# Performance work log

Measured on AMD Instinct MI355X. Metric: run time of the kernel, lower is better.

Reference implementation:

```python
import jax, jax.numpy as jnp
import numpy as np

NH = 8  # num_heads


def _conv1x1(w, b, x):
    # 1x1 conv == channel matmul: w [O,C], x [B,C,H,W]
    return jnp.einsum('oc,bchw->bohw', w, x) + b[None, :, None, None]


def _fwd(low_freq_feat, high_freq_feat, ext_context, road_feat,
         ext_proj_w, ext_proj_b, road_proj_w, road_proj_b,
         ext_qkv_w, ext_qkv_b, road_qkv_w, road_qkv_b,
         ext_out_w, ext_out_b, road_out_w, road_out_b,
         gate_ext_w, gate_ext_b, gate_road_w, gate_road_b):
    B, C, H, W = low_freq_feat.shape
    nh = NH
    hd = C // nh
    HW = H * W
    scale = hd ** -0.5

    ext_p = ext_context @ ext_proj_w.T + ext_proj_b          # [B,C]
    road_p = _conv1x1(road_proj_w, road_proj_b, road_feat)   # [B,C,H,W]

    eqkv = (ext_p @ ext_qkv_w.T + ext_qkv_b).reshape(B, 3, nh, hd)
    ext_q, ext_v = eqkv[:, 0], eqkv[:, 2]                    # [B,nh,hd]

    # torch: conv out [B,3C,H,W] viewed as (B,C,3,H,W) -> q/k/v interleaved over channels
    rqkv = _conv1x1(road_qkv_w, road_qkv_b, road_p).reshape(B, C, 3, H, W)
    road_k = rqkv[:, :, 1].reshape(B, nh, hd, HW).transpose(0, 1, 3, 2)  # [B,nh,HW,hd]
    road_v = rqkv[:, :, 2].reshape(B, nh, hd, HW).transpose(0, 1, 3, 2)

    # ext->road attention. The torch code expands ext_q to HW identical rows; one row
    # per (batch, head) gives a bit-identical result without the [B,nh,HW,HW] blowup.
    scores = jnp.einsum('bnd,bnpd->bnp', ext_q, road_k) * scale
    attn = jax.nn.softmax(scores, axis=-1)                   # [B,nh,HW]
    ext_head = jnp.einsum('bnp,bnpd->bnd', attn, road_v).reshape(B, C)
    ext_vec = ext_head @ ext_out_w.T + ext_out_b             # [B,C]
    ext_feat_spatial = jnp.broadcast_to(ext_vec[:, :, None, None], (B, C, H, W))

    # road->ext attention: all HW keys/values are copies of the single ext token, so
    # softmax is exactly uniform and the output per position is exactly ext_v. The
    # road_out 1x1 conv on a spatially-constant map is a single matvec per batch.
    road_vec = ext_v.reshape(B, C) @ road_out_w.T + road_out_b
    road_enhanced = jnp.broadcast_to(road_vec[:, :, None, None], (B, C, H, W))

    # gated fusion (ext stream): spatial mean of constant map == ext_vec
    gate_in = jnp.concatenate([low_freq_feat.mean(axis=(2, 3)), ext_vec], axis=-1)
    ext_gate = jax.nn.sigmoid(gate_in @ gate_ext_w.T + gate_ext_b)[:, :, None, None]
    ext_final = low_freq_feat * (1.0 - ext_gate) + ext_feat_spatial * ext_gate

    # gated fusion (road stream)
    rg_in = jnp.concatenate([high_freq_feat, road_enhanced], axis=1)  # [B,2C,H,W]
    road_gate = jax.nn.sigmoid(_conv1x1(gate_road_w, gate_road_b, rg_in))
    road_final = high_freq_feat * (1.0 - road_gate) + road_enhanced * road_gate
    return ext_final, road_final


def setup_inputs() -> dict:
    key = jax.random.key(0)
    ks = jax.random.split(key, 20)
    B, C, H, W, E = 8, 256, 64, 64, 64
    f = lambda k, shape, s=1.0: jax.random.normal(k, shape, dtype=jnp.float32) * s
    return {
        'low_freq_feat': f(ks[0], (B, C, H, W)),
        'high_freq_feat': f(ks[1], (B, C, H, W)),
        'ext_context': f(ks[2], (B, E)),
        'road_feat': f(ks[3], (B, C, H, W)),
        'ext_proj_w': f(ks[4], (C, E), 0.05), 'ext_proj_b': f(ks[5], (C,), 0.02),
        'road_proj_w': f(ks[6], (C, C), 0.05), 'road_proj_b': f(ks[7], (C,), 0.02),
        'ext_qkv_w': f(ks[8], (3 * C, C), 0.05), 'ext_qkv_b': f(ks[9], (3 * C,), 0.02),
        'road_qkv_w': f(ks[10], (3 * C, C), 0.05), 'road_qkv_b': f(ks[11], (3 * C,), 0.02),
        'ext_out_w': f(ks[12], (C, C), 0.05), 'ext_out_b': f(ks[13], (C,), 0.02),
        'road_out_w': f(ks[14], (C, C), 0.05), 'road_out_b': f(ks[15], (C,), 0.02),
        'gate_ext_w': f(ks[16], (C, 2 * C), 0.05), 'gate_ext_b': f(ks[17], (C,), 0.02),
        'gate_road_w': f(ks[18], (C, 2 * C), 0.05), 'gate_road_b': f(ks[19], (C,), 0.02),
    }


def reference(low_freq_feat, high_freq_feat, ext_context, road_feat,
              ext_proj_w, ext_proj_b, road_proj_w, road_proj_b,
              ext_qkv_w, ext_qkv_b, road_qkv_w, road_qkv_b,
              ext_out_w, ext_out_b, road_out_w, road_out_b,
              gate_ext_w, gate_ext_b, gate_road_w, gate_road_b):
    return _fwd(low_freq_feat, high_freq_feat, ext_context, road_feat,
                ext_proj_w, ext_proj_b, road_proj_w, road_proj_b,
                ext_qkv_w, ext_qkv_b, road_qkv_w, road_qkv_b,
                ext_out_w, ext_out_b, road_out_w, road_out_b,
                gate_ext_w, gate_ext_b, gate_road_w, gate_road_b)
```

## Files before the change

kernel.cpp:

```cpp
#include <hip/hip_runtime.h>

typedef short bf16x8 __attribute__((ext_vector_type(8)));
typedef float f32x4 __attribute__((ext_vector_type(4)));

#define ATT_SCALE 0.17677669529663687f

__device__ __forceinline__ unsigned short f2b(float f) {
    unsigned int u = __builtin_bit_cast(unsigned int, f);
    unsigned int r = u + 0x7FFFu + ((u >> 16) & 1u);
    return (unsigned short)(r >> 16);
}
__device__ __forceinline__ float b2f(unsigned short v) {
    return __builtin_bit_cast(float, (unsigned int)v << 16);
}
__device__ __forceinline__ float wsum64(float v) {
    #pragma unroll
    for (int m = 32; m; m >>= 1) v += __shfl_xor(v, m, 64);
    return v;
}


__global__ __launch_bounds__(256) void k_setup(const float* __restrict__ w1,
                                               const float* __restrict__ wqkv,
                                               const float* __restrict__ b1,
                                               const float* __restrict__ bqkv,
                                               const float* __restrict__ gate_road_w,
                                               const float* __restrict__ ext_proj_w,
                                               const float* __restrict__ ext_qkv_w,
                                               const float* __restrict__ road_out_w,
                                               const float* __restrict__ ext_out_w,
                                               const float* __restrict__ gate_ext_w,
                                               const float* __restrict__ low,
                                               unsigned short* __restrict__ W3b,
                                               unsigned short* __restrict__ Wcb,
                                               unsigned short* __restrict__ WF,
                                               float* __restrict__ bcv,
                                               float* __restrict__ mean_low) {
    int bid = blockIdx.x, t = threadIdx.x;
    __shared__ float sel[8][256];
    __shared__ float red[8][4];
    if (bid >= 448) {
        int bc = bid - 448;
        const f32x4* p4 = (const f32x4*)(low + (size_t)bc * 4096);
        float s = 0.f;
        for (int i = t; i < 1024; i += 256) {
            f32x4 v = p4[i];
            s += v[0] + v[1] + v[2] + v[3];
        }
        s = wsum64(s);
        if ((t & 63) == 0) red[0][t >> 6] = s;
        __syncthreads();
        if (t == 0) mean_low[bc] = (red[0][0] + red[0][1] + red[0][2] + red[0][3]) * (1.0f / 4096.0f);
    } else if (bid < 256) {
        int i = bid * 256 + t;
        int o = i >> 8, k = i & 255;
        W3b[i] = f2b(gate_road_w[o * 512 + k]);
    } else if (bid < 320) {
        int o0 = (bid - 256) * 8;
        #pragma unroll
        for (int r = 0; r < 8; r++) {
            int o = o0 + r;
            int c = (o < 256) ? o : o - 256;
            int g = (o < 256) ? 1 : 2;
            sel[r][t] = wqkv[(size_t)(3 * c + g) * 256 + t];
        }
        __syncthreads();
        float b1v = b1[t];
        #pragma unroll
        for (int r = 0; r < 8; r++) {
            float v = wsum64(sel[r][t] * b1v);
            if ((t & 63) == 0) red[r][t >> 6] = v;
        }
        __syncthreads();
        if (t < 8) {
            int o = o0 + t;
            int c = (o < 256) ? o : o - 256;
            int g = (o < 256) ? 1 : 2;
            bcv[o] = red[t][0] + red[t][1] + red[t][2] + red[t][3] + bqkv[3 * c + g];
        }
        float acc[8] = {};
        #pragma unroll 16
        for (int m = 0; m < 256; m++) {
            float w1v = w1[(size_t)m * 256 + t];
            #pragma unroll
            for (int r = 0; r < 8; r++) acc[r] += sel[r][m] * w1v;
        }
        #pragma unroll
        for (int r = 0; r < 8; r++) Wcb[(size_t)(o0 + r) * 256 + t] = f2b(acc[r]);
    } else {
        int mb = bid - 320;
        int m = mb >> 4, ctile = mb & 15;
        const float* src;
        int stride, K, coff;
        unsigned short* dst;
        switch (m) {
        case 0: src = ext_qkv_w;                     stride = 256; K = 256; coff = 0;   dst = WF;          break;
        case 1: src = ext_qkv_w + (size_t)512 * 256; stride = 256; K = 256; coff = 0;   dst = WF + 65536;  break;
        case 2: src = road_out_w;                    stride = 256; K = 256; coff = 0;   dst = WF + 131072; break;
        case 3: src = gate_road_w;                   stride = 512; K = 256; coff = 256; dst = WF + 196608; break;
        case 4: src = ext_proj_w;                    stride = 64;  K = 64;  coff = 0;   dst = WF + 262144; break;
        case 5: src = ext_out_w;                     stride = 256; K = 256; coff = 0;   dst = WF + 278528; break;
        case 6: src = gate_ext_w;                    stride = 512; K = 256; coff = 0;   dst = WF + 344064; break;
        default: src = gate_ext_w;                   stride = 512; K = 256; coff = 256; dst = WF + 409600; break;
        }
        int lc = t >> 4, kseg = t & 15;
        int k0 = kseg * 16;
        if (k0 < K) {
            int c = ctile * 16 + lc;
            const float* sp = src + (size_t)c * stride + coff + k0;
            f32x4 v0 = *(const f32x4*)sp;
            f32x4 v1 = *(const f32x4*)(sp + 4);
            f32x4 v2 = *(const f32x4*)(sp + 8);
            f32x4 v3 = *(const f32x4*)(sp + 12);
            int kk = kseg >> 1;
            int Kt = K >> 5;
            #pragma unroll
            for (int h = 0; h < 2; h++) {
                int lhi = (kseg & 1) * 2 + h;
                int lane = lhi * 16 + lc;
                bf16x8 o;
                f32x4 a = h ? v2 : v0, b = h ? v3 : v1;
                #pragma unroll
                for (int i = 0; i < 4; i++) { o[i] = (short)f2b(a[i]); o[4 + i] = (short)f2b(b[i]); }
                *(bf16x8*)(dst + ((size_t)(ctile * Kt + kk) << 9) + lane * 8) = o;
            }
        }
    }
}

__global__ __launch_bounds__(256) void k_tiny(const unsigned short* __restrict__ WF,
                                              const float* __restrict__ ext_context,
                                              const float* __restrict__ ext_proj_b,
                                              const float* __restrict__ ext_qkv_b,
                                              const float* __restrict__ road_out_b,
                                              const float* __restrict__ gate_road_b,
                                              float* __restrict__ ext_q,
                                              float* __restrict__ road_vec,
                                              float* __restrict__ rg_const) {
    __shared__ unsigned short xA[16][264];
    __shared__ unsigned short xB[16][264];
    int t = threadIdx.x;
    int w = t >> 6, lane = t & 63, l15 = lane & 15, lhi = lane >> 4;
    const unsigned short* WqF  = WF;
    const unsigned short* WvF  = WF + 65536;
    const unsigned short* WroF = WF + 131072;
    const unsigned short* WgF  = WF + 196608;
    const unsigned short* WpF  = WF + 262144;
    {
        int b = t >> 5, k0 = (t & 31) * 2;
        float c0v = ext_context[b * 64 + k0];
        float c1v = ext_context[b * 64 + k0 + 1];
        *(unsigned int*)&xA[b][k0] = (unsigned int)f2b(c0v) | ((unsigned int)f2b(c1v) << 16);
    }
    __syncthreads();
    {
        f32x4 acc[4] = {};
        #pragma unroll
        for (int kk = 0; kk < 2; kk++) {
            bf16x8 a = *(const bf16x8*)&xA[l15][kk * 32 + 8 * lhi];
            #pragma unroll
            for (int ni = 0; ni < 4; ni++) {
                int ct = w * 4 + ni;
                bf16x8 bfr = *(const bf16x8*)(WpF + ((size_t)(ct * 2 + kk) << 9) + lane * 8);
                acc[ni] = __builtin_amdgcn_mfma_f32_16x16x32_bf16(a, bfr, acc[ni], 0, 0, 0);
            }
        }
        if (lhi < 2) {
            #pragma unroll
            for (int ni = 0; ni < 4; ni++) {
                int c = w * 64 + ni * 16 + l15;
                float bp = ext_proj_b[c];
                #pragma unroll
                for (int r = 0; r < 4; r++)
                    xB[4 * lhi + r][c] = f2b(acc[ni][r] + bp);
            }
        }
    }
    __syncthreads();
    {
        f32x4 acc[8] = {};
        bool isq = (w < 2);
        int cbase = (w & 1) * 128;
        const unsigned short* Wb = isq ? WqF : WvF;
        for (int kk = 0; kk < 8; kk++) {
            bf16x8 a = *(const bf16x8*)&xB[l15][kk * 32 + 8 * lhi];
            #pragma unroll
            for (int ni = 0; ni < 8; ni++) {
                int ct = (cbase >> 4) + ni;
                bf16x8 bfr = *(const bf16x8*)(Wb + ((size_t)(ct * 8 + kk) << 9) + lane * 8);
                acc[ni] = __builtin_amdgcn_mfma_f32_16x16x32_bf16(a, bfr, acc[ni], 0, 0, 0);
            }
        }
        if (lhi < 2) {
            #pragma unroll
            for (int ni = 0; ni < 8; ni++) {
                int c = cbase + ni * 16 + l15;
                float bb = ext_qkv_b[(isq ? 0 : 512) + c];
                #pragma unroll
                for (int r = 0; r < 4; r++) {
                    int b = 4 * lhi + r;
                    float val = acc[ni][r] + bb;
                    if (isq) ext_q[b * 256 + c] = val;
                    else     xA[b][c] = f2b(val);
                }
            }
        }
    }
    __syncthreads();
    {
        f32x4 acc[4] = {};
        for (int kk = 0; kk < 8; kk++) {
            bf16x8 a = *(const bf16x8*)&xA[l15][kk * 32 + 8 * lhi];
            #pragma unroll
            for (int ni = 0; ni < 4; ni++) {
                int ct = w * 4 + ni;
                bf16x8 bfr = *(const bf16x8*)(WroF + ((size_t)(ct * 8 + kk) << 9) + lane * 8);
                acc[ni] = __builtin_amdgcn_mfma_f32_16x16x32_bf16(a, bfr, acc[ni], 0, 0, 0);
            }
        }
        if (lhi < 2) {
            #pragma unroll
            for (int ni = 0; ni < 4; ni++) {
                int c = w * 64 + ni * 16 + l15;
                float bb = road_out_b[c];
                #pragma unroll
                for (int r = 0; r < 4; r++) {
                    int b = 4 * lhi + r;
                    float val = acc[ni][r] + bb;
                    road_vec[b * 256 + c] = val;
                    xB[b][c] = f2b(val);
                }
            }
        }
    }
    __syncthreads();
    {
        f32x4 acc[4] = {};
        for (int kk = 0; kk < 8; kk++) {
            bf16x8 a = *(const bf16x8*)&xB[l15][kk * 32 + 8 * lhi];
            #pragma unroll
            for (int ni = 0; ni < 4; ni++) {
                int ct = w * 4 + ni;
                bf16x8 bfr = *(const bf16x8*)(WgF + ((size_t)(ct * 8 + kk) << 9) + lane * 8);
                acc[ni] = __builtin_amdgcn_mfma_f32_16x16x32_bf16(a, bfr, acc[ni], 0, 0, 0);
            }
        }
        if (lhi < 2) {
            #pragma unroll
            for (int ni = 0; ni < 4; ni++) {
                int c = w * 64 + ni * 16 + l15;
                float bb = gate_road_b[c];
                #pragma unroll
                for (int r = 0; r < 4; r++)
                    rg_const[(4 * lhi + r) * 256 + c] = acc[ni][r] + bb;
            }
        }
    }
}

__global__ __launch_bounds__(256) void k_qfold(const unsigned short* __restrict__ Wcb,
                                               const float* __restrict__ bcv,
                                               const float* __restrict__ ext_q,
                                               unsigned short* __restrict__ wqf,
                                               float* __restrict__ cqs) {
    int b = blockIdx.x, t = threadIdx.x;
    __shared__ float qs[256];
    __shared__ float wq[8][256];
    qs[t] = ext_q[b * 256 + t];
    __syncthreads();
    float acc[8] = {};
    #pragma unroll
    for (int h = 0; h < 8; h++)
        #pragma unroll 8
        for (int d = 0; d < 32; d++)
            acc[h] += qs[h * 32 + d] * b2f(Wcb[(size_t)(h * 32 + d) * 256 + t]);
    #pragma unroll
    for (int h = 0; h < 8; h++) wq[h][t] = acc[h];
    if (t < 8) {
        float s = 0.f;
        #pragma unroll 8
        for (int d = 0; d < 32; d++) s += qs[t * 32 + d] * bcv[t * 32 + d];
        cqs[b * 8 + t] = s * ATT_SCALE;
    }
    __syncthreads();
    #pragma unroll
    for (int q2 = 0; q2 < 2; q2++) {
        int idx = t + 256 * q2;
        int kk = idx >> 6, l = idx & 63;
        int row = l & 15;
        int kb = kk * 32 + (l >> 4) * 8;
        bf16x8 o;
        #pragma unroll
        for (int e = 0; e < 8; e++)
            o[e] = (row < 8) ? (short)f2b(wq[row][kb + e]) : (short)0;
        *(bf16x8*)(wqf + ((size_t)(b * 8 + kk) * 64 + l) * 8) = o;
    }
}

__global__ __launch_bounds__(256) void k_att(const float* __restrict__ road_feat,
                                             const unsigned short* __restrict__ wqf,
                                             const float* __restrict__ cqs,
                                             float* __restrict__ part) {
    __shared__ unsigned short Xs[32 * 256];
    __shared__ unsigned short Xt[256][40];
    __shared__ float es_[8][36];
    __shared__ float Yl[256 * 12];
    char* Xc = (char*)Xs;
    int bid = blockIdx.x;
    int b  = bid >> 7;
    int p0 = (bid & 127) << 5;
    int t  = threadIdx.x;
    const float* rfb = road_feat + (size_t)b * 1048576;

    int c0 = 2 * (t >> 3);
    int j4 = (t & 7) * 4;
    #pragma unroll
    for (int it = 0; it < 4; ++it) {
        int c = c0 + 64 * it;
        f32x4 g0 = *(const f32x4*)(rfb + (size_t)c * 4096 + p0 + j4);
        f32x4 g1 = *(const f32x4*)(rfb + (size_t)(c + 1) * 4096 + p0 + j4);
        unsigned short h0[4], h1[4];
        #pragma unroll
        for (int i = 0; i < 4; i++) { h0[i] = f2b(g0[i]); h1[i] = f2b(g1[i]); }
        #pragma unroll
        for (int i = 0; i < 4; i++) {
            int j = j4 + i;
            unsigned int pk = (unsigned int)h0[i] | ((unsigned int)h1[i] << 16);
            *(unsigned int*)(Xc + ((j * 512 + 2 * c) ^ ((j & 15) << 4))) = pk;
        }
        *(unsigned int*)&Xt[c][j4]         = (unsigned int)h0[0] | ((unsigned int)h0[1] << 16);
        *(unsigned int*)&Xt[c][j4 + 2]     = (unsigned int)h0[2] | ((unsigned int)h0[3] << 16);
        *(unsigned int*)&Xt[c + 1][j4]     = (unsigned int)h1[0] | ((unsigned int)h1[1] << 16);
        *(unsigned int*)&Xt[c + 1][j4 + 2] = (unsigned int)h1[2] | ((unsigned int)h1[3] << 16);
    }
    __syncthreads();

    int w = t >> 6, lane = t & 63, l15 = lane & 15, lhi = lane >> 4;

    if (w < 2) {
        f32x4 acc = {};
        int px = w * 16 + l15;
        for (int kk = 0; kk < 8; kk++) {
            bf16x8 aq = *(const bf16x8*)(wqf + ((size_t)(b * 8 + kk) * 64 + lane) * 8);
            bf16x8 bx = *(const bf16x8*)(Xc + ((px * 512 + (kk * 32 + 8 * lhi) * 2) ^ ((px & 15) << 4)));
            acc = __builtin_amdgcn_mfma_f32_16x16x32_bf16(aq, bx, acc, 0, 0, 0);
        }
        #pragma unroll
        for (int r = 0; r < 4; r++) {
            int row = 4 * lhi + r;
            if (row < 8)
                es_[row][w * 16 + l15] = expf(acc[r] * ATT_SCALE + cqs[b * 8 + row]);
        }
    }
    __syncthreads();

    float* pb = part + (size_t)bid * 2056;
    {
        float v = es_[t >> 5][t & 31];
        v += __shfl_xor(v, 1, 64);
        v += __shfl_xor(v, 2, 64);
        v += __shfl_xor(v, 4, 64);
        v += __shfl_xor(v, 8, 64);
        v += __shfl_xor(v, 16, 64);
        if ((lane & 31) == 0) pb[t >> 5] = v;
    }
    bf16x8 besv;
    {
        f32x4 e0 = *(const f32x4*)&es_[l15 & 7][8 * lhi];
        f32x4 e1 = *(const f32x4*)&es_[l15 & 7][8 * lhi + 4];
        #pragma unroll
        for (int i = 0; i < 4; i++) { besv[i] = (short)f2b(e0[i]); besv[4 + i] = (short)f2b(e1[i]); }
    }
    #pragma unroll
    for (int mf = 0; mf < 4; mf++) {
        int f = w * 4 + mf;
        int c = f * 16 + l15;
        bf16x8 ax = *(const bf16x8*)&Xt[c][8 * lhi];
        f32x4 acc = {};
        acc = __builtin_amdgcn_mfma_f32_16x16x32_bf16(ax, besv, acc, 0, 0, 0);
        if (l15 < 8) {
            #pragma unroll
            for (int r = 0; r < 4; r++)
                Yl[(f * 16 + 4 * lhi + r) * 12 + l15] = acc[r];
        }
    }
    __syncthreads();
    {
        f32x4 y0, y1;
        #pragma unroll
        for (int i = 0; i < 4; i++) { y0[i] = Yl[t * 12 + i]; y1[i] = Yl[t * 12 + 4 + i]; }
        *(f32x4*)(pb + 8 + t * 8)     = y0;
        *(f32x4*)(pb + 8 + t * 8 + 4) = y1;
    }
}

__global__ __launch_bounds__(256) void k_red(const float* __restrict__ part,
                                             float* __restrict__ part2) {
    int blk = blockIdx.x, t = threadIdx.x;
    int base = blk * 8;
    float acc[8] = {};
    float accS = 0.f;
    #pragma unroll
    for (int g = 0; g < 8; g++) {
        const float* pb = part + (size_t)(base + g) * 2056;
        #pragma unroll
        for (int i = 0; i < 8; i++) acc[i] += pb[8 + 256 * i + t];
        if (t < 8) accS += pb[t];
    }
    float* ob = part2 + (size_t)blk * 2056;
    if (t < 8) ob[t] = accS;
    #pragma unroll
    for (int i = 0; i < 8; i++) ob[8 + 256 * i + t] = acc[i];
}

__global__ __launch_bounds__(256) void k_comb(const float* __restrict__ part2,
                                              const unsigned short* __restrict__ Wcb,
                                              const float* __restrict__ bcv,
                                              float* __restrict__ hdg) {
    int b = blockIdx.x, t = threadIdx.x;
    __shared__ float Yt[8][260];
    __shared__ float S[8];
    const float* pbase = part2 + (size_t)b * 16 * 2056;
    float acc[8] = {};
    float accS = 0.f;
    #pragma unroll 4
    for (int g = 0; g < 16; g++) {
        const float* pb = pbase + (size_t)g * 2056;
        #pragma unroll
        for (int i = 0; i < 8; i++) acc[i] += pb[8 + 256 * i + t];
        if (t < 8) accS += pb[t];
    }
    #pragma unroll
    for (int i = 0; i < 8; i++) {
        int e = 256 * i + t;
        Yt[e & 7][e >> 3] = acc[i];
    }
    if (t < 8) S[t] = accS;
    __syncthreads();

    int w = t >> 6, lane = t & 63, l15 = lane & 15, lhi = lane >> 4;
    float invS = 1.0f / S[l15 & 7];
    #pragma unroll
    for (int mf = 0; mf < 4; mf++) {
        int f = w * 4 + mf;
        f32x4 acc4 = {};
        for (int kk = 0; kk < 8; kk++) {
            bf16x8 aw = *(const bf16x8*)(Wcb + (size_t)(256 + f * 16 + l15) * 256 + kk * 32 + 8 * lhi);
            f32x4 y0 = *(const f32x4*)&Yt[l15 & 7][kk * 32 + 8 * lhi];
            f32x4 y1 = *(const f32x4*)&Yt[l15 & 7][kk * 32 + 8 * lhi + 4];
            bf16x8 by;
            #pragma unroll
            for (int i = 0; i < 4; i++) { by[i] = (short)f2b(y0[i]); by[4 + i] = (short)f2b(y1[i]); }
            acc4 = __builtin_amdgcn_mfma_f32_16x16x32_bf16(aw, by, acc4, 0, 0, 0);
        }
        if (l15 == (f >> 1)) {
            #pragma unroll
            for (int r = 0; r < 4; r++) {
                int row = f * 16 + 4 * lhi + r;
                hdg[b * 256 + row] = acc4[r] * invS + bcv[256 + row];
            }
        }
    }
}

__global__ __launch_bounds__(256) void k_vec2(const unsigned short* __restrict__ WF,
                                              const float* __restrict__ hdg,
                                              const float* __restrict__ mean_low,
                                              const float* __restrict__ ext_out_b,
                                              const float* __restrict__ gate_ext_b,
                                              float* __restrict__ ext_vec,
                                              float* __restrict__ ext_gate) {
    __shared__ unsigned short xA[16][264];
    __shared__ unsigned short xB[16][264];
    __shared__ unsigned short xC[16][264];
    int t = threadIdx.x;
    int w = t >> 6, lane = t & 63, l15 = lane & 15, lhi = lane >> 4;
    const unsigned short* WoF    = WF + 278528;
    const unsigned short* WgeLoF = WF + 344064;
    const unsigned short* WgeHiF = WF + 409600;
    {
        int bb = t >> 5, kb = t & 31;
        #pragma unroll
        for (int q = 0; q < 4; q++) {
            int k0 = (kb + 32 * q) * 2;
            *(unsigned int*)&xA[bb][k0] =
                (unsigned int)f2b(hdg[bb * 256 + k0]) | ((unsigned int)f2b(hdg[bb * 256 + k0 + 1]) << 16);
            *(unsigned int*)&xB[bb][k0] =
                (unsigned int)f2b(mean_low[bb * 256 + k0]) | ((unsigned int)f2b(mean_low[bb * 256 + k0 + 1]) << 16);
        }
    }
    __syncthreads();
    {
        f32x4 acc[4] = {};
        for (int kk = 0; kk < 8; kk++) {
            bf16x8 a = *(const bf16x8*)&xA[l15][kk * 32 + 8 * lhi];
            #pragma unroll
            for (int ni = 0; ni < 4; ni++) {
                int ct = w * 4 + ni;
                bf16x8 bfr = *(const bf16x8*)(WoF + ((size_t)(ct * 8 + kk) << 9) + lane * 8);
                acc[ni] = __builtin_amdgcn_mfma_f32_16x16x32_bf16(a, bfr, acc[ni], 0, 0, 0);
            }
        }
        if (lhi < 2) {
            #pragma unroll
            for (int ni = 0; ni < 4; ni++) {
                int c = w * 64 + ni * 16 + l15;
                float bb = ext_out_b[c];
                #pragma unroll
                for (int r = 0; r < 4; r++) {
                    int b = 4 * lhi + r;
                    float val = acc[ni][r] + bb;
                    ext_vec[b * 256 + c] = val;
                    xC[b][c] = f2b(val);
                }
            }
        }
    }
    __syncthreads();
    {
        f32x4 acc[4] = {};
        for (int kk = 0; kk < 8; kk++) {
            bf16x8 a = *(const bf16x8*)&xB[l15][kk * 32 + 8 * lhi];
            #pragma unroll
            for (int ni = 0; ni < 4; ni++) {
                int ct = w * 4 + ni;
                bf16x8 bfr = *(const bf16x8*)(WgeLoF + ((size_t)(ct * 8 + kk) << 9) + lane * 8);
                acc[ni] = __builtin_amdgcn_mfma_f32_16x16x32_bf16(a, bfr, acc[ni], 0, 0, 0);
            }
        }
        for (int kk = 0; kk < 8; kk++) {
            bf16x8 a = *(const bf16x8*)&xC[l15][kk * 32 + 8 * lhi];
            #pragma unroll
            for (int ni = 0; ni < 4; ni++) {
                int ct = w * 4 + ni;
                bf16x8 bfr = *(const bf16x8*)(WgeHiF + ((size_t)(ct * 8 + kk) << 9) + lane * 8);
                acc[ni] = __builtin_amdgcn_mfma_f32_16x16x32_bf16(a, bfr, acc[ni], 0, 0, 0);
            }
        }
        if (lhi < 2) {
            #pragma unroll
            for (int ni = 0; ni < 4; ni++) {
                int c = w * 64 + ni * 16 + l15;
                float bb = gate_ext_b[c];
                #pragma unroll
                for (int r = 0; r < 4; r++) {
                    int b = 4 * lhi + r;
                    ext_gate[b * 256 + c] = 1.0f / (1.0f + expf(-(acc[ni][r] + bb)));
                }
            }
        }
    }
}

__global__ __launch_bounds__(256) void k_ext_final(const float* __restrict__ low,
                                                   const float* __restrict__ ext_vec,
                                                   const float* __restrict__ ext_gate,
                                                   float* __restrict__ out) {
    int idx = blockIdx.x * 256 + threadIdx.x;
    #pragma unroll
    for (int rep = 0; rep < 4; ++rep) {
        int i = idx + rep * 524288;
        int bc = i >> 10;
        float g = ext_gate[bc];
        float vv = ext_vec[bc];
        f32x4 L = *(const f32x4*)(low + (size_t)i * 4);
        f32x4 o;
        #pragma unroll
        for (int c = 0; c < 4; c++) o[c] = L[c] + g * (vv - L[c]);
        *(f32x4*)(out + (size_t)i * 4) = o;
    }
}

__global__ __launch_bounds__(512) void k_road(const float* __restrict__ high,
                                              const unsigned short* __restrict__ W3b,
                                              const float* __restrict__ rg_const,
                                              const float* __restrict__ road_vec,
                                              float* __restrict__ outbuf) {
    __shared__ float Xs[32 * 256];
    char* Xc = (char*)Xs;
    int bid = blockIdx.x;
    int b  = bid >> 7;
    int p0 = (bid & 127) << 5;
    int t  = threadIdx.x;
    const float* hb = high + (size_t)b * 1048576;

    int c0 = t >> 3;
    int j4 = (t & 7) * 4;
    #pragma unroll
    for (int it = 0; it < 4; ++it) {
        int c = c0 + 64 * it;
        f32x4 g = *(const f32x4*)(hb + (size_t)c * 4096 + p0 + j4);
        #pragma unroll
        for (int i = 0; i < 4; i++) {
            int j = j4 + i;
            *(float*)(Xc + ((j * 1024 + 4 * c) ^ ((j & 15) << 4))) = g[i];
        }
    }
    __syncthreads();

    int w = t >> 6, lane = t & 63, l15 = lane & 15, lhi = lane >> 4;
    f32x4 acc[2][2] = {};
    for (int kk = 0; kk < 8; kk++) {
        bf16x8 a[2];
        #pragma unroll
        for (int mi = 0; mi < 2; mi++) {
            int j = mi * 16 + l15;
            int base = j * 1024 + (kk * 32 + 8 * lhi) * 4;
            int sw = (j & 15) << 4;
            f32x4 x0 = *(const f32x4*)(Xc + (base ^ sw));
            f32x4 x1 = *(const f32x4*)(Xc + ((base + 16) ^ sw));
            bf16x8 av;
            #pragma unroll
            for (int i = 0; i < 4; i++) {
                av[i]     = (short)f2b(x0[i]);
                av[4 + i] = (short)f2b(x1[i]);
            }
            a[mi] = av;
        }
        #pragma unroll
        for (int ni = 0; ni < 2; ni++) {
            int o = w * 32 + ni * 16 + l15;
            bf16x8 bf = *(const bf16x8*)(W3b + (size_t)o * 256 + kk * 32 + 8 * lhi);
            acc[0][ni] = __builtin_amdgcn_mfma_f32_16x16x32_bf16(a[0], bf, acc[0][ni], 0, 0, 0);
            acc[1][ni] = __builtin_amdgcn_mfma_f32_16x16x32_bf16(a[1], bf, acc[1][ni], 0, 0, 0);
        }
    }
    __syncthreads();

    #pragma unroll
    for (int ni = 0; ni < 2; ni++) {
        int o = w * 32 + ni * 16 + l15;
        float rc = rg_const[b * 256 + o];
        float rv = road_vec[b * 256 + o];
        #pragma unroll
        for (int mi = 0; mi < 2; mi++)
            #pragma unroll
            for (int r = 0; r < 4; r++) {
                int j = mi * 16 + 4 * lhi + r;
                float* slot = (float*)(Xc + ((j * 1024 + 4 * o) ^ ((j & 15) << 4)));
                float z = acc[mi][ni][r] + rc;
                float gte = 1.0f / (1.0f + expf(-z));
                float hv = *slot;
                *slot = hv + gte * (rv - hv);
            }
    }
    __syncthreads();

    float* ob = outbuf + 8388608 + (size_t)b * 1048576;
    #pragma unroll
    for (int it = 0; it < 4; ++it) {
        int c = c0 + 64 * it;
        f32x4 o4;
        #pragma unroll
        for (int i = 0; i < 4; i++) {
            int j = j4 + i;
            o4[i] = *(const float*)(Xc + ((j * 1024 + 4 * c) ^ ((j & 15) << 4)));
        }
        *(f32x4*)(ob + (size_t)c * 4096 + p0 + j4) = o4;
    }
}

extern "C" void kernel_launch(void* const* d_in, const int* in_sizes, int n_in,
                              void* d_out, int out_size, void* d_ws, size_t ws_size,
                              hipStream_t stream) {
    const float* low         = (const float*)d_in[0];
    const float* high        = (const float*)d_in[1];
    const float* ext_context = (const float*)d_in[2];
    const float* road_feat   = (const float*)d_in[3];
    const float* ext_proj_w  = (const float*)d_in[4];
    const float* ext_proj_b  = (const float*)d_in[5];
    const float* road_proj_w = (const float*)d_in[6];
    const float* road_proj_b = (const float*)d_in[7];
    const float* ext_qkv_w   = (const float*)d_in[8];
    const float* ext_qkv_b   = (const float*)d_in[9];
    const float* road_qkv_w  = (const float*)d_in[10];
    const float* road_qkv_b  = (const float*)d_in[11];
    const float* ext_out_w   = (const float*)d_in[12];
    const float* ext_out_b   = (const float*)d_in[13];
    const float* road_out_w  = (const float*)d_in[14];
    const float* road_out_b  = (const float*)d_in[15];
    const float* gate_ext_w  = (const float*)d_in[16];
    const float* gate_ext_b  = (const float*)d_in[17];
    const float* gate_road_w = (const float*)d_in[18];
    const float* gate_road_b = (const float*)d_in[19];

    float* out = (float*)d_out;
    unsigned short* wsb = (unsigned short*)d_ws;
    unsigned short* Wcb = wsb;
    unsigned short* W3b = wsb + 131072;
    float* fw = (float*)((char*)d_ws + 983040);
    float* ext_q    = fw;
    float* road_vec = fw + 2048;
    float* rg_const = fw + 4096;
    float* ext_vec  = fw + 8192;
    float* ext_gate = fw + 10240;
    float* mean_low = fw + 12288;
    float* bcv      = fw + 14336;
    float* hdg      = fw + 16384;
    float* cqs      = fw + 18432;
    unsigned short* wqf = (unsigned short*)(fw + 18496);
    float* part  = out + 2097152;
    float* part2 = out + 4718592;
    unsigned short* WF = (unsigned short*)(out + 5242880);

    k_setup<<<2496, 256, 0, stream>>>(road_proj_w, road_qkv_w, road_proj_b, road_qkv_b,
                                      gate_road_w, ext_proj_w, ext_qkv_w, road_out_w,
                                      ext_out_w, gate_ext_w, low,
                                      W3b, Wcb, WF, bcv, mean_low);
    k_tiny<<<1, 256, 0, stream>>>(WF, ext_context, ext_proj_b, ext_qkv_b,
                                  road_out_b, gate_road_b, ext_q, road_vec, rg_const);
    k_qfold<<<8, 256, 0, stream>>>(Wcb, bcv, ext_q, wqf, cqs);
    k_att<<<1024, 256, 0, stream>>>(road_feat, wqf, cqs, part);
    k_red<<<128, 256, 0, stream>>>(part, part2);
    k_comb<<<8, 256, 0, stream>>>(part2, Wcb, bcv, hdg);
    k_vec2<<<1, 256, 0, stream>>>(WF, hdg, mean_low, ext_out_b, gate_ext_b,
                                  ext_vec, ext_gate);
    k_ext_final<<<2048, 256, 0, stream>>>(low, ext_vec, ext_gate, out);
    k_road<<<1024, 512, 0, stream>>>(high, W3b, rg_const, road_vec, out);
}
```

Baseline: 149.0 us.

## Shrink k_road tiles to 16 positions and alias k_att shared buffers

k_road now runs 2048 blocks of 256 threads, each handling 16 spatial positions instead of 32, with each wave covering 64 output channels over a single M tile. This halves the LDS footprint per block so more blocks can be resident per CU. k_att aliases its Yl scratch onto the Xs staging buffer to cut LDS use and raise occupancy. The trade-off is that each W3b fragment loaded from global memory is reused across fewer positions, so weight traffic per output goes up.

```diff
diff --git a/kernel.cpp b/kernel.cpp
--- a/kernel.cpp
+++ b/kernel.cpp
@@ -301,11 +301,11 @@
                                              const unsigned short* __restrict__ wqf,
                                              const float* __restrict__ cqs,
                                              float* __restrict__ part) {
-    __shared__ unsigned short Xs[32 * 256];
+    __shared__ __align__(16) char u_smem[32 * 256 * 2];
     __shared__ unsigned short Xt[256][40];
     __shared__ float es_[8][36];
-    __shared__ float Yl[256 * 12];
-    char* Xc = (char*)Xs;
+    char* Xc = u_smem;
+    float* Yl = (float*)u_smem;
     int bid = blockIdx.x;
     int b  = bid >> 7;
     int p0 = (bid & 127) << 5;
@@ -571,21 +571,21 @@
     }
 }
 
-__global__ __launch_bounds__(512) void k_road(const float* __restrict__ high,
+__global__ __launch_bounds__(256) void k_road(const float* __restrict__ high,
                                               const unsigned short* __restrict__ W3b,
                                               const float* __restrict__ rg_const,
                                               const float* __restrict__ road_vec,
                                               float* __restrict__ outbuf) {
-    __shared__ float Xs[32 * 256];
+    __shared__ float Xs[16 * 256];
     char* Xc = (char*)Xs;
     int bid = blockIdx.x;
-    int b  = bid >> 7;
-    int p0 = (bid & 127) << 5;
+    int b  = bid >> 8;
+    int p0 = (bid & 255) << 4;
     int t  = threadIdx.x;
     const float* hb = high + (size_t)b * 1048576;
 
-    int c0 = t >> 3;
-    int j4 = (t & 7) * 4;
+    int c0 = t >> 2;
+    int j4 = (t & 3) * 4;
     #pragma unroll
     for (int it = 0; it < 4; ++it) {
         int c = c0 + 64 * it;
@@ -599,50 +599,41 @@
     __syncthreads();
 
     int w = t >> 6, lane = t & 63, l15 = lane & 15, lhi = lane >> 4;
-    f32x4 acc[2][2] = {};
+    f32x4 acc[4] = {};
     for (int kk = 0; kk < 8; kk++) {
-        bf16x8 a[2];
-        #pragma unroll
-        for (int mi = 0; mi < 2; mi++) {
-            int j = mi * 16 + l15;
-            int base = j * 1024 + (kk * 32 + 8 * lhi) * 4;
-            int sw = (j & 15) << 4;
-            f32x4 x0 = *(const f32x4*)(Xc + (base ^ sw));
-            f32x4 x1 = *(const f32x4*)(Xc + ((base + 16) ^ sw));
-            bf16x8 av;
-            #pragma unroll
-            for (int i = 0; i < 4; i++) {
-                av[i]     = (short)f2b(x0[i]);
-                av[4 + i] = (short)f2b(x1[i]);
-            }
-            a[mi] = av;
-        }
-        #pragma unroll
-        for (int ni = 0; ni < 2; ni++) {
-            int o = w * 32 + ni * 16 + l15;
+        int base = (kk * 32 + 8 * lhi) * 4;
+        int sw = l15 << 4;
+        f32x4 x0 = *(const f32x4*)(Xc + ((l15 * 1024 + base) ^ sw));
+        f32x4 x1 = *(const f32x4*)(Xc + ((l15 * 1024 + base + 16) ^ sw));
+        bf16x8 av;
+        #pragma unroll
+        for (int i = 0; i < 4; i++) {
+            av[i]     = (short)f2b(x0[i]);
+            av[4 + i] = (short)f2b(x1[i]);
+        }
+        #pragma unroll
+        for (int ni = 0; ni < 4; ni++) {
+            int o = w * 64 + ni * 16 + l15;
             bf16x8 bf = *(const bf16x8*)(W3b + (size_t)o * 256 + kk * 32 + 8 * lhi);
-            acc[0][ni] = __builtin_amdgcn_mfma_f32_16x16x32_bf16(a[0], bf, acc[0][ni], 0, 0, 0);
-            acc[1][ni] = __builtin_amdgcn_mfma_f32_16x16x32_bf16(a[1], bf, acc[1][ni], 0, 0, 0);
-        }
-    }
-    __syncthreads();
-
-    #pragma unroll
-    for (int ni = 0; ni < 2; ni++) {
-        int o = w * 32 + ni * 16 + l15;
+            acc[ni] = __builtin_amdgcn_mfma_f32_16x16x32_bf16(av, bf, acc[ni], 0, 0, 0);
+        }
+    }
+    __syncthreads();
+
+    #pragma unroll
+    for (int ni = 0; ni < 4; ni++) {
+        int o = w * 64 + ni * 16 + l15;
         float rc = rg_const[b * 256 + o];
         float rv = road_vec[b * 256 + o];
         #pragma unroll
-        for (int mi = 0; mi < 2; mi++)
-            #pragma unroll
-            for (int r = 0; r < 4; r++) {
-                int j = mi * 16 + 4 * lhi + r;
-                float* slot = (float*)(Xc + ((j * 1024 + 4 * o) ^ ((j & 15) << 4)));
-                float z = acc[mi][ni][r] + rc;
-                float gte = 1.0f / (1.0f + expf(-z));
-                float hv = *slot;
-                *slot = hv + gte * (rv - hv);
-            }
+        for (int r = 0; r < 4; r++) {
+            int j = 4 * lhi + r;
+            float* slot = (float*)(Xc + ((j * 1024 + 4 * o) ^ ((j & 15) << 4)));
+            float z = acc[ni][r] + rc;
+            float gte = 1.0f / (1.0f + expf(-z));
+            float hv = *slot;
+            *slot = hv + gte * (rv - hv);
+        }
     }
     __syncthreads();
 
@@ -716,5 +707,5 @@
     k_vec2<<<1, 256, 0, stream>>>(WF, hdg, mean_low, ext_out_b, gate_ext_b,
                                   ext_vec, ext_gate);
     k_ext_final<<<2048, 256, 0, stream>>>(low, ext_vec, ext_gate, out);
-    k_road<<<1024, 512, 0, stream>>>(high, W3b, rg_const, road_vec, out);
-}
+    k_road<<<2048, 256, 0, stream>>>(high, W3b, rg_const, road_vec, out);
+}
```

Result: slower. 164.7 us (+10.6%).
